# Optimization experiments

Measured on AMD Instinct MI355X. Metric: run time of the kernel, lower is better.

The kernel has to match this reference:

```python
import jax, jax.numpy as jnp
import numpy as np

B, N, C, NQ, DK = 4, 4096, 256, 14, 512
REG, N_ITER = 0.05, 100


def l2norm(x):
    n = jnp.linalg.norm(x, axis=-1, keepdims=True)
    return x / jnp.maximum(n, 1e-12)  # F.normalize(p=2, eps=1e-12)


def sinkhorn(a, b, M, reg=REG, n_iter=N_ITER):
    # a: [B,n] source marginal, b: [B,m] target marginal, M: [B,n,m] cost.
    K = jnp.exp(-M / reg)
    u0 = jnp.ones_like(a) / a.shape[-1]
    v0 = jnp.ones_like(b) / b.shape[-1]
    def step(carry, _):
        u, v = carry
        v = b / (jnp.einsum('bnm,bn->bm', K, u) + 1e-16)
        u = a / (jnp.einsum('bnm,bm->bn', K, v) + 1e-16)
        return (u, v), None
    (u, v), _ = jax.lax.scan(step, (u0, v0), None, length=n_iter)
    return u[:, :, None] * K * v[:, None, :]  # [B,n,m]


def setup_inputs() -> dict:
    key = jax.random.key(0)
    ks = jax.random.split(key, 20)
    s = 0.02
    f32 = jnp.float32
    return {
        'q': jax.random.normal(ks[0], (B, N, C), f32),
        'k': jax.random.normal(ks[1], (B, N, C), f32),
        'v': jax.random.normal(ks[2], (B, N, C), f32),
        'seed_vector': jax.random.normal(ks[3], (B, C, NQ), f32),
        'supp_valid_mask': jax.random.randint(ks[4], (B, N), 0, 2, jnp.int32),
        'supp_mask': jax.random.randint(ks[5], (B, N), 0, 2, jnp.int32),
        'Wq': jax.random.normal(ks[6], (C, C), f32) * s,
        'Wk': jax.random.normal(ks[7], (C, C), f32) * s,
        'Wv': jax.random.normal(ks[8], (C, C), f32) * s,
        'Ws': jax.random.normal(ks[9], (C, C), f32) * s,
        'Wsq': jax.random.normal(ks[10], (C, C), f32) * s,
        'Wsk': jax.random.normal(ks[11], (C, C), f32) * s,
        'Wproj': jax.random.normal(ks[12], (C, C), f32) * s,
        'Wqs': jax.random.normal(ks[13], (C, DK), f32) * s,
        'Wks': jax.random.normal(ks[14], (C, DK), f32) * s,
        'Wvs': jax.random.normal(ks[15], (C, DK), f32) * s,
        'Wfc': jax.random.normal(ks[16], (DK, C), f32) * s,
        'bfc': jnp.zeros((C,), f32),
        'ln_g': jnp.ones((C,), f32),
        'ln_b': jnp.zeros((C,), f32),
    }


def reference(q, k, v, seed_vector, supp_valid_mask, supp_mask,
              Wq, Wk, Wv, Ws, Wsq, Wsk, Wproj, Wqs, Wks, Wvs, Wfc, bfc, ln_g, ln_b):
    # ---- input projections (eval mode: all dropouts are identity) ----
    qs = q @ Wq                                   # [B,N,C]
    kk = k @ Wk                                   # [B,N,C]
    vv = v @ Wv                                   # [B,N,C]
    seed = jnp.einsum('bcq,cd->bqd', seed_vector, Ws)  # s_fc(seed.permute) -> [B,NQ,C]

    # ---- MultiHeadAttentionOne (n_head=1, d_k=d_v=512) ----
    qh = seed @ Wqs                               # [B,NQ,DK]
    kh = kk @ Wks                                 # [B,N,DK]
    vh = vv @ Wvs                                 # [B,N,DK]
    logits = jnp.einsum('bqd,bnd->bqn', qh, kh) / jnp.sqrt(jnp.float32(DK))
    logits = jnp.where(supp_mask[:, None, :] == 0, jnp.float32(-1e9), logits)
    A = jax.nn.softmax(logits, axis=-1)
    ctx = jnp.einsum('bqn,bnd->bqd', A, vh) @ Wfc + bfc  # [B,NQ,C]
    pre = ctx + seed                              # residual
    mu = jnp.mean(pre, axis=-1, keepdims=True)
    var = jnp.var(pre, axis=-1, keepdims=True)
    prototypes = (pre - mu) / jnp.sqrt(var + 1e-5) * ln_g + ln_b  # [B,NQ,C]

    pk = prototypes @ Wsk                         # seed_k_fc
    pq = prototypes @ Wsq                         # seed_q_fc

    # ---- cosine similarity q->prototypes ----
    att_q2p = jnp.einsum('bnc,bkc->bnk', l2norm(qs), l2norm(pk))  # [B,N,NQ]

    # ---- OT-enhanced similarity supp->prototypes ----
    att = jnp.einsum('bnc,bkc->bnk', l2norm(kk), l2norm(pq))      # [B,N,NQ]
    num_bg = jnp.sum((supp_mask == 0).astype(jnp.float32), axis=-1, keepdims=True)  # [B,1]
    num_fg = jnp.float32(N) - num_bg
    trash = jnp.where((supp_mask > 0)[:, :, None], jnp.float32(2.0), jnp.float32(0.0))  # [B,N,1]
    cost = jnp.concatenate([1.0 - att, trash], axis=2)            # [B,N,NQ+1]
    col = jnp.full((B, N), 1.0 / N, dtype=jnp.float32)
    row = jnp.concatenate([jnp.broadcast_to(num_fg / NQ, (B, NQ)), num_bg], axis=1) / N
    T = sinkhorn(col, row, cost) * N
    att_s2p = jax.nn.relu(T[:, :, :-1])                           # [B,N,NQ]

    sid_s = jnp.argmax(att_s2p, axis=2)                           # [B,N] int
    sid_q = jnp.argmax(att_q2p, axis=2)                           # [B,N] int

    attn = jnp.einsum('bnk,bmk->bnm', att_q2p, att_s2p)           # [B,Nq,Nk]

    # ---- align mask (vectorized form of the per-batch loop) ----
    align = jnp.sqrt((sid_s.astype(jnp.float32) + 1.5)[:, :, None] *
                     (sid_q.astype(jnp.float32) + 1.5)[:, None, :])  # [B,Nk,Nq]
    not_align = jnp.where((2.0 * align) % 1.0 == 0.0, 0.0, 1.0)
    not_align = jnp.transpose(not_align, (0, 2, 1))               # [B,Nq,Nk]

    attn = attn + supp_valid_mask[:, None, :].astype(jnp.float32) * (-10000.0)
    attn = attn + not_align * (-10000.0)
    attn = jax.nn.softmax(attn, axis=-1)
    x = (attn @ vv) @ Wproj                                       # [B,N,C]
    return x
```

## Files before the change

### kernel.cpp

```cpp
#include <hip/hip_runtime.h>
#include <math.h>

#define NB 4
#define NN 4096
#define NC 256
#define NQ 14

typedef __attribute__((ext_vector_type(8))) short short8;
typedef __attribute__((ext_vector_type(4))) float f32x4;
typedef _Float16 f16x8 __attribute__((ext_vector_type(8)));
union UH8 { uint4 u4; f16x8 h8; _Float16 h[8]; };

__device__ __forceinline__ float blockReduceSum256(float v, float* sred) {
    #pragma unroll
    for (int off = 32; off; off >>= 1) v += __shfl_xor(v, off, 64);
    const int lane = threadIdx.x & 63, wid = threadIdx.x >> 6;
    if (lane == 0) sred[wid] = v;
    __syncthreads();
    float s = sred[0] + sred[1] + sred[2] + sred[3];
    __syncthreads();
    return s;
}

__device__ __forceinline__ float dpp_wave_sum63(float x) {
    x += __int_as_float(__builtin_amdgcn_update_dpp(0, __float_as_int(x), 0x111, 0xf, 0xf, true));
    x += __int_as_float(__builtin_amdgcn_update_dpp(0, __float_as_int(x), 0x112, 0xf, 0xf, true));
    x += __int_as_float(__builtin_amdgcn_update_dpp(0, __float_as_int(x), 0x114, 0xf, 0xf, true));
    x += __int_as_float(__builtin_amdgcn_update_dpp(0, __float_as_int(x), 0x118, 0xf, 0xf, true));
    x += __int_as_float(__builtin_amdgcn_update_dpp(0, __float_as_int(x), 0x142, 0xf, 0xf, true));
    x += __int_as_float(__builtin_amdgcn_update_dpp(0, __float_as_int(x), 0x143, 0xf, 0xf, true));
    return x;
}
__device__ __forceinline__ float rdlane(float x, int l) {
    return __int_as_float(__builtin_amdgcn_readlane(__float_as_int(x), l));
}

__global__ __launch_bounds__(256) void gemm_aw(const float* __restrict__ A,
                                               const float* __restrict__ W,
                                               float* __restrict__ out) {
    const int t = threadIdx.x;
    const int row0 = blockIdx.y * 64;
    const int cb = blockIdx.x * 128;
    __shared__ __align__(16) float Ast[32][68];
    __shared__ __align__(16) float Wt[32][132];
    const int r0 = (t & 15) * 4;
    const int c0 = (t >> 4) * 8;
    const int ar = t >> 2;
    const int ak = (t & 3) * 8;
    const int wr = t >> 3;
    const int wc = (t & 7) * 16;
    float acc[4][8];
    #pragma unroll
    for (int i = 0; i < 4; i++)
        #pragma unroll
        for (int j = 0; j < 8; j++) acc[i][j] = 0.f;

    for (int k0 = 0; k0 < 256; k0 += 32) {
        const float* asrc = A + (size_t)(row0 + ar) * 256 + k0 + ak;
        float4 a0 = *(const float4*)asrc;
        float4 a1 = *(const float4*)(asrc + 4);
        const float* wsrc = W + (size_t)(k0 + wr) * 256 + cb + wc;
        float4 w0 = *(const float4*)wsrc;
        float4 w1 = *(const float4*)(wsrc + 4);
        float4 w2 = *(const float4*)(wsrc + 8);
        float4 w3 = *(const float4*)(wsrc + 12);
        __syncthreads();
        Ast[ak + 0][ar] = a0.x; Ast[ak + 1][ar] = a0.y;
        Ast[ak + 2][ar] = a0.z; Ast[ak + 3][ar] = a0.w;
        Ast[ak + 4][ar] = a1.x; Ast[ak + 5][ar] = a1.y;
        Ast[ak + 6][ar] = a1.z; Ast[ak + 7][ar] = a1.w;
        *(float4*)&Wt[wr][wc + 0] = w0;
        *(float4*)&Wt[wr][wc + 4] = w1;
        *(float4*)&Wt[wr][wc + 8] = w2;
        *(float4*)&Wt[wr][wc + 12] = w3;
        __syncthreads();
        #pragma unroll
        for (int kk = 0; kk < 32; kk++) {
            const float4 a4 = *(const float4*)&Ast[kk][r0];
            const float4 wa = *(const float4*)&Wt[kk][c0];
            const float4 wb = *(const float4*)&Wt[kk][c0 + 4];
            const float av[4] = {a4.x, a4.y, a4.z, a4.w};
            const float wv[8] = {wa.x, wa.y, wa.z, wa.w, wb.x, wb.y, wb.z, wb.w};
            #pragma unroll
            for (int i = 0; i < 4; i++)
                #pragma unroll
                for (int j = 0; j < 8; j++) acc[i][j] += av[i] * wv[j];
        }
    }
    #pragma unroll
    for (int i = 0; i < 4; i++) {
        float* dst = out + (size_t)(row0 + r0 + i) * 256 + cb + c0;
        *(float4*)dst = make_float4(acc[i][0], acc[i][1], acc[i][2], acc[i][3]);
        *(float4*)(dst + 4) = make_float4(acc[i][4], acc[i][5], acc[i][6], acc[i][7]);
    }
}

__global__ __launch_bounds__(256) void prep_wqk(const float* __restrict__ Wqs,
                                                const float* __restrict__ Wks,
                                                float* __restrict__ Wqk2) {
    __shared__ __align__(16) float srow[512];
    const int c1 = blockIdx.x, c2 = threadIdx.x;
    srow[c2] = Wqs[c1 * 512 + c2];
    srow[c2 + 256] = Wqs[c1 * 512 + 256 + c2];
    __syncthreads();
    const float* wk = Wks + (size_t)c2 * 512;
    float acc = 0.f;
    for (int d = 0; d < 512; d += 4) {
        float4 a = *(const float4*)&srow[d];
        float4 b = *(const float4*)(wk + d);
        acc += a.x * b.x + a.y * b.y + a.z * b.z + a.w * b.w;
    }
    Wqk2[c1 * 256 + c2] = acc * 0.044194173824159216f;
}

__global__ __launch_bounds__(256) void prep_wcomb(const float* __restrict__ Wvs,
                                                  const float* __restrict__ Wfc,
                                                  float* __restrict__ Wcomb) {
    __shared__ float srow[512];
    const int c1 = blockIdx.x, c2 = threadIdx.x;
    srow[c2] = Wvs[c1 * 512 + c2];
    srow[c2 + 256] = Wvs[c1 * 512 + 256 + c2];
    __syncthreads();
    float acc = 0.f;
    for (int d = 0; d < 512; d++) acc += srow[d] * Wfc[d * 256 + c2];
    Wcomb[c1 * 256 + c2] = acc;
}

__global__ __launch_bounds__(256) void k_seed(const float* __restrict__ sv,
                                              const float* __restrict__ Ws,
                                              const float* __restrict__ Wqk2,
                                              float* __restrict__ seed,
                                              float* __restrict__ qhk) {
    const int q = blockIdx.x, b = blockIdx.y, c = threadIdx.x;
    __shared__ float ssv[256];
    __shared__ float sseed[256];
    ssv[c] = sv[((size_t)b * 256 + c) * 14 + q];
    __syncthreads();
    float acc = 0.f;
    for (int d = 0; d < 256; d++) acc += ssv[d] * Ws[d * 256 + c];
    seed[((size_t)b * 14 + q) * 256 + c] = acc;
    sseed[c] = acc;
    __syncthreads();
    float a2 = 0.f;
    for (int d = 0; d < 256; d++) a2 += sseed[d] * Wqk2[d * 256 + c];
    qhk[((size_t)b * 14 + q) * 256 + c] = a2;
}

__global__ __launch_bounds__(256) void k_vvhalf(const float* __restrict__ vv,
                                                _Float16* __restrict__ vvT_h) {
    __shared__ float tile[64][65];
    const int b = blockIdx.z, c0 = blockIdx.y * 64, m0 = blockIdx.x * 64;
    const int t = threadIdx.x;
    #pragma unroll
    for (int i = 0; i < 4; i++) {
        const int m = (t >> 4) + i * 16;
        const float4 v4 = *(const float4*)(vv + ((size_t)b * 4096 + m0 + m) * 256 + c0 + (t & 15) * 4);
        tile[(t & 15) * 4 + 0][m] = v4.x;
        tile[(t & 15) * 4 + 1][m] = v4.y;
        tile[(t & 15) * 4 + 2][m] = v4.z;
        tile[(t & 15) * 4 + 3][m] = v4.w;
    }
    __syncthreads();
    const int c = t >> 2, mo = (t & 3) * 16;
    UH8 o0, o1;
    #pragma unroll
    for (int j = 0; j < 8; j++) {
        o0.h[j] = (_Float16)tile[c][mo + j];
        o1.h[j] = (_Float16)tile[c][mo + 8 + j];
    }
    const size_t off = ((size_t)b * 256 + c0 + c) * 4096 + m0 + mo;
    *(uint4*)(vvT_h + off) = o0.u4;
    *(uint4*)(vvT_h + off + 8) = o1.u4;
}

__global__ __launch_bounds__(256) void k_logits1(const float* __restrict__ kk,
                                                 const float* __restrict__ qhk,
                                                 const int* __restrict__ supp,
                                                 float* __restrict__ logits) {
    const int b = blockIdx.y;
    const int n = blockIdx.x * 256 + threadIdx.x;
    __shared__ __align__(16) float sq[14][256];
    for (int i = threadIdx.x; i < 14 * 256; i += 256) sq[i >> 8][i & 255] = qhk[b * 14 * 256 + i];
    __syncthreads();
    float acc[14];
    #pragma unroll
    for (int q = 0; q < 14; q++) acc[q] = 0.f;
    const float* krow = kk + ((size_t)b * 4096 + n) * 256;
    for (int c = 0; c < 256; c += 4) {
        const float4 k4 = *(const float4*)(krow + c);
        #pragma unroll
        for (int q = 0; q < 14; q++) {
            const float4 a4 = *(const float4*)&sq[q][c];
            acc[q] += k4.x * a4.x + k4.y * a4.y + k4.z * a4.z + k4.w * a4.w;
        }
    }
    const bool msk = (supp[b * 4096 + n] == 0);
    #pragma unroll
    for (int q = 0; q < 14; q++)
        logits[((size_t)b * 14 + q) * 4096 + n] = msk ? -1e9f : acc[q];
}

__global__ __launch_bounds__(256) void k_softmax1(float* __restrict__ logits) {
    const int b = blockIdx.y, qq = blockIdx.x, t = threadIdx.x;
    __shared__ __align__(16) float sl[4096];
    __shared__ float sred[8];
    float* row = logits + ((size_t)b * 14 + qq) * 4096;
    float mx = -3e38f;
    for (int i = t; i < 4096; i += 256) { float v = row[i]; sl[i] = v; mx = fmaxf(mx, v); }
    #pragma unroll
    for (int off = 32; off; off >>= 1) mx = fmaxf(mx, __shfl_xor(mx, off, 64));
    if ((t & 63) == 0) sred[t >> 6] = mx;
    __syncthreads();
    mx = fmaxf(fmaxf(sred[0], sred[1]), fmaxf(sred[2], sred[3]));
    __syncthreads();
    float s = 0.f;
    for (int i = t; i < 4096; i += 256) { float e = expf(sl[i] - mx); sl[i] = e; s += e; }
    #pragma unroll
    for (int off = 32; off; off >>= 1) s += __shfl_xor(s, off, 64);
    if ((t & 63) == 0) sred[t >> 6] = s;
    __syncthreads();
    s = sred[0] + sred[1] + sred[2] + sred[3];
    const float inv = 1.f / s;
    for (int i = t; i < 4096; i += 256) row[i] = sl[i] * inv;
}

__global__ __launch_bounds__(256) void k_ctxv(const float* __restrict__ A,
                                              const float* __restrict__ vv,
                                              float* __restrict__ part) {
    const int b = blockIdx.y, ch = blockIdx.x, c = threadIdx.x;
    const int n0 = ch * 256;
    __shared__ __align__(16) float sA[14][256];
    for (int i = c; i < 14 * 256; i += 256) {
        int qq = i >> 8, j = i & 255;
        sA[qq][j] = A[((size_t)b * 14 + qq) * 4096 + n0 + j];
    }
    __syncthreads();
    float acc[14];
    #pragma unroll
    for (int q = 0; q < 14; q++) acc[q] = 0.f;
    for (int n = 0; n < 256; n += 4) {
        const float v0 = vv[((size_t)b * 4096 + n0 + n + 0) * 256 + c];
        const float v1 = vv[((size_t)b * 4096 + n0 + n + 1) * 256 + c];
        const float v2 = vv[((size_t)b * 4096 + n0 + n + 2) * 256 + c];
        const float v3 = vv[((size_t)b * 4096 + n0 + n + 3) * 256 + c];
        #pragma unroll
        for (int q = 0; q < 14; q++) {
            const float4 a4 = *(const float4*)&sA[q][n];
            acc[q] += a4.x * v0 + a4.y * v1 + a4.z * v2 + a4.w * v3;
        }
    }
    #pragma unroll
    for (int q = 0; q < 14; q++) part[(((size_t)b * 16 + ch) * 14 + q) * 256 + c] = acc[q];
}

__global__ __launch_bounds__(256) void k_proto(const float* __restrict__ part,
                                               const float* __restrict__ Wcomb,
                                               const float* __restrict__ bfc,
                                               const float* __restrict__ seed,
                                               const float* __restrict__ lng,
                                               const float* __restrict__ lnb,
                                               const float* __restrict__ Wsk,
                                               const float* __restrict__ Wsq,
                                               float* __restrict__ pkn,
                                               float* __restrict__ pqn) {
    const int q = blockIdx.x, b = blockIdx.y, c = threadIdx.x;
    __shared__ float sctx[256];
    __shared__ float sproto[256];
    __shared__ float sred[8];
    float cv = 0.f;
    for (int ch = 0; ch < 16; ch++) cv += part[(((size_t)b * 16 + ch) * 14 + q) * 256 + c];
    sctx[c] = cv;
    __syncthreads();
    float pre = 0.f;
    for (int d = 0; d < 256; d++) pre += sctx[d] * Wcomb[d * 256 + c];
    pre += bfc[c] + seed[((size_t)b * 14 + q) * 256 + c];
    const float mu = blockReduceSum256(pre, sred) * (1.f / 256.f);
    const float dv = pre - mu;
    const float var = blockReduceSum256(dv * dv, sred) * (1.f / 256.f);
    const float proto = dv * (1.f / sqrtf(var + 1e-5f)) * lng[c] + lnb[c];
    sproto[c] = proto;
    __syncthreads();
    float pk = 0.f, pq = 0.f;
    for (int d = 0; d < 256; d++) {
        const float sp = sproto[d];
        pk += sp * Wsk[d * 256 + c];
        pq += sp * Wsq[d * 256 + c];
    }
    const float nk = blockReduceSum256(pk * pk, sred);
    const float nq = blockReduceSum256(pq * pq, sred);
    pkn[((size_t)b * 14 + q) * 256 + c] = pk / fmaxf(sqrtf(nk), 1e-12f);
    pqn[((size_t)b * 14 + q) * 256 + c] = pq / fmaxf(sqrtf(nq), 1e-12f);
}

__global__ __launch_bounds__(256) void k_q2p(const float* __restrict__ qs,
                                             const float* __restrict__ kk,
                                             const float* __restrict__ pkn,
                                             const float* __restrict__ pqn,
                                             float* __restrict__ aq2p,
                                             float* __restrict__ attc,
                                             int* __restrict__ sidq) {
    const int b = blockIdx.y;
    const int n = blockIdx.x * 256 + threadIdx.x;
    __shared__ __align__(16) float spk[14][256];
    __shared__ __align__(16) float spq[14][256];
    for (int i = threadIdx.x; i < 14 * 256; i += 256) {
        spk[i >> 8][i & 255] = pkn[b * 14 * 256 + i];
        spq[i >> 8][i & 255] = pqn[b * 14 * 256 + i];
    }
    __syncthreads();
    float aq[14], ak[14];
    #pragma unroll
    for (int q = 0; q < 14; q++) { aq[q] = 0.f; ak[q] = 0.f; }
    float nq = 0.f, nk = 0.f;
    const float* qrow = qs + ((size_t)b * 4096 + n) * 256;
    const float* krow = kk + ((size_t)b * 4096 + n) * 256;
    for (int c = 0; c < 256; c += 4) {
        const float4 q4 = *(const float4*)(qrow + c);
        const float4 k4 = *(const float4*)(krow + c);
        nq += q4.x * q4.x + q4.y * q4.y + q4.z * q4.z + q4.w * q4.w;
        nk += k4.x * k4.x + k4.y * k4.y + k4.z * k4.z + k4.w * k4.w;
        #pragma unroll
        for (int q = 0; q < 14; q++) {
            const float4 p4 = *(const float4*)&spk[q][c];
            const float4 p4b = *(const float4*)&spq[q][c];
            aq[q] += q4.x * p4.x + q4.y * p4.y + q4.z * p4.z + q4.w * p4.w;
            ak[q] += k4.x * p4b.x + k4.y * p4b.y + k4.z * p4b.z + k4.w * p4b.w;
        }
    }
    const float sq_ = 1.f / fmaxf(sqrtf(nq), 1e-12f);
    const float sk_ = 1.f / fmaxf(sqrtf(nk), 1e-12f);
    float* aqrow = aq2p + ((size_t)b * 4096 + n) * 14;
    float* akrow = attc + ((size_t)b * 4096 + n) * 14;
    int best = 0;
    float bv = -3e38f;
    #pragma unroll
    for (int q = 0; q < 14; q++) {
        const float v = aq[q] * sq_;
        aqrow[q] = v;
        if (v > bv) { bv = v; best = q; }
        akrow[q] = ak[q] * sk_;
    }
    sidq[b * 4096 + n] = best;
}

__global__ __launch_bounds__(512, 1) void k_sinkhorn(const float* __restrict__ attc,
                                                     const int* __restrict__ supp,
                                                     const int* __restrict__ valid,
                                                     _Float16* __restrict__ as2ph,
                                                     int* __restrict__ code) {
    const int b = blockIdx.x;
    const int t = threadIdx.x;
    const int lane = t & 63, wid = t >> 6;
    __shared__ __align__(16) float wred[2][15][8];
    __shared__ float sbg[8];
    float K[8][15], u[8];
    float bgcnt = 0.f;
    #pragma unroll
    for (int j = 0; j < 8; j++) {
        const int n = t + j * 512;
        const int sm = supp[b * 4096 + n];
        bgcnt += (sm == 0) ? 1.f : 0.f;
        const float* arow = attc + ((size_t)b * 4096 + n) * 14;
        #pragma unroll
        for (int m = 0; m < 14; m++) K[j][m] = expf(-20.f * (1.f - arow[m]));
        K[j][14] = (sm > 0) ? expf(-40.f) : 1.f;
        u[j] = 1.f / 4096.f;
    }
    #pragma unroll
    for (int j = 0; j < 8; j++)
        #pragma unroll
        for (int m = 0; m < 15; m++)
            asm volatile("" : "+v"(K[j][m]));
    const float bgw = dpp_wave_sum63(bgcnt);
    if (lane == 63) sbg[wid] = bgw;
    __syncthreads();
    float num_bg = 0.f;
    #pragma unroll
    for (int w = 0; w < 8; w++) num_bg += sbg[w];
    const float num_fg = 4096.f - num_bg;
    const float bm_fg = num_fg / (14.f * 4096.f);
    const float bm_tr = num_bg / 4096.f;
    const float a_n = 1.f / 4096.f;
    const float mybm = (lane < 14) ? bm_fg : bm_tr;

    float vloc[15];
    for (int it = 0; it < 100; it++) {
        const int buf = it & 1;
        float tot[15];
        #pragma unroll
        for (int m = 0; m < 15; m++) {
            float s = 0.f;
            #pragma unroll
            for (int j = 0; j < 8; j++) s += K[j][m] * u[j];
            tot[m] = rdlane(dpp_wave_sum63(s), 63);
        }
        float wv = 0.f;
        #pragma unroll
        for (int m = 0; m < 15; m++) wv = (lane == m) ? tot[m] : wv;
        if (lane < 15) wred[buf][lane][wid] = wv;
        __syncthreads();
        float vtmp = 0.f;
        {
            const float4 r0 = *(const float4*)&wred[buf][lane < 15 ? lane : 0][0];
            const float4 r1 = *(const float4*)&wred[buf][lane < 15 ? lane : 0][4];
            const float s = r0.x + r0.y + r0.z + r0.w + r1.x + r1.y + r1.z + r1.w;
            vtmp = mybm * __builtin_amdgcn_rcpf(s + 1e-16f);
        }
        #pragma unroll
        for (int m = 0; m < 15; m++) vloc[m] = rdlane(vtmp, m);
        #pragma unroll
        for (int j = 0; j < 8; j++) {
            float s = 0.f;
            #pragma unroll
            for (int m = 0; m < 15; m++) s += K[j][m] * vloc[m];
            u[j] = a_n * __builtin_amdgcn_rcpf(s + 1e-16f);
        }
    }
    #pragma unroll
    for (int j = 0; j < 8; j++) {
        const int n = t + j * 512;
        float bv = -3e38f;
        int bi = 0;
        union { uint4 u4[4]; _Float16 h[32]; } ob;
        #pragma unroll
        for (int m = 0; m < 14; m++) {
            const float tv = fmaxf(4096.f * u[j] * K[j][m] * vloc[m], 0.f);
            const _Float16 hh = (_Float16)tv;
            ob.h[m] = hh;
            ob.h[16 + m] = (_Float16)(tv - (float)hh);
            if (tv > bv) { bv = tv; bi = m; }
        }
        ob.h[14] = (_Float16)0.f; ob.h[15] = (_Float16)0.f;
        ob.h[30] = (_Float16)0.f; ob.h[31] = (_Float16)0.f;
        uint4* dst = (uint4*)(as2ph + ((size_t)(b * 4096 + n)) * 32);
        dst[0] = ob.u4[0]; dst[1] = ob.u4[1];
        dst[2] = ob.u4[2]; dst[3] = ob.u4[3];
        int msk = 1 << bi;
        if (bi == 0) msk |= (1 << 12);
        else if (bi == 12) msk |= 1;
        else if (bi == 3) msk |= (1 << 11);
        else if (bi == 11) msk |= (1 << 3);
        code[b * 4096 + n] = msk | (valid[b * 4096 + n] << 14);
    }
}

__global__ __launch_bounds__(256) void k_lamtab(const int* __restrict__ code,
                                                int* __restrict__ lamtab) {
    const int b = blockIdx.x, t = threadIdx.x;
    __shared__ int sm0[4], sm1[4];
    int m0 = 0, m1 = 0;
    for (int m = t; m < 4096; m += 256) {
        const int c = code[b * 4096 + m];
        const int mask = c & 0x3fff;
        const int v = c >> 14;
        const int nmask = (~mask) & 0x3fff;
        if (v == 0) { m0 |= mask; m1 |= nmask; }
        else { m1 |= mask; }
    }
    #pragma unroll
    for (int off = 32; off; off >>= 1) {
        m0 |= __shfl_xor(m0, off, 64);
        m1 |= __shfl_xor(m1, off, 64);
    }
    if ((t & 63) == 0) { sm0[t >> 6] = m0; sm1[t >> 6] = m1; }
    __syncthreads();
    if (t == 0) {
        lamtab[b * 2 + 0] = sm0[0] | sm0[1] | sm0[2] | sm0[3];
        lamtab[b * 2 + 1] = sm1[0] | sm1[1] | sm1[2] | sm1[3];
    }
}

__global__ __launch_bounds__(512, 2) void k_fused(const float* __restrict__ aq2p,
                                                  const _Float16* __restrict__ as2ph,
                                                  const int* __restrict__ code,
                                                  const int* __restrict__ sidq,
                                                  const int* __restrict__ lamtab,
                                                  const _Float16* __restrict__ vvT_h,
                                                  float* __restrict__ y) {
    const int bid = blockIdx.x;
    const int xcd = bid & 7, slot = bid >> 3;
    const int b = xcd >> 1;
    const int n0 = ((xcd & 1) * 64 + slot) * 32;
    const int t = threadIdx.x;
    const int l = t & 63, wv = t >> 6;
    const int wn = wv & 1, wcS = wv >> 1;
    const int quad = l >> 4, lr = l & 15;

    __shared__ __align__(16) _Float16 Pl[2][32 * 128];
    __shared__ float rsl[4][32];
    __shared__ int ssq[32], sml[32];
    __shared__ float rinv_s[32];

    if (t < 32) {
        const int sq = sidq[b * 4096 + n0 + t];
        const int lm0 = lamtab[b * 2], lm1 = lamtab[b * 2 + 1];
        ssq[t] = sq;
        sml[t] = ((lm0 >> sq) & 1) ? 0 : (((lm1 >> sq) & 1) ? 1 : 2);
    }
    __syncthreads();
    int sqp = 0;
    #pragma unroll
    for (int r = 0; r < 4; r++) {
        const int row_l = wn * 16 + quad * 4 + r;
        sqp |= (ssq[row_l] & 31) << (r * 8);
        sqp |= (sml[row_l] & 3) << (r * 8 + 5);
    }
    UH8 a1, a2;
    {
        const float* arow = aq2p + ((size_t)(b * 4096 + n0 + wn * 16 + lr)) * 14;
        const int kb = (quad & 1) * 8;
        #pragma unroll
        for (int j = 0; j < 8; j++) {
            const int kk2 = kb + j;
            const float f = (kk2 < 14) ? arow[kk2] : 0.f;
            const _Float16 hi = (_Float16)f;
            a1.h[j] = hi;
            a2.h[j] = (quad < 2) ? (_Float16)(f - (float)hi) : (_Float16)0.f;
        }
    }
    const _Float16* a2base = as2ph + (size_t)b * 4096 * 32 + quad * 8;
    const int* cbase = code + b * 4096;
    const _Float16* bvb0 = vvT_h + ((size_t)(b * 256 + wv * 32 + lr)) * 4096 + quad * 8;
    const _Float16* bvb1 = bvb0 + (size_t)16 * 4096;

    UH8 bS[2];
    int cdr[2];
    #pragma unroll
    for (int i = 0; i < 2; i++) {
        const int m = (wcS * 2 + i) * 16 + lr;
        bS[i].u4 = *(const uint4*)(a2base + (size_t)m * 32);
        cdr[i] = cbase[m];
    }
    UH8 bA[8], bB[8];
    #pragma unroll
    for (int ms = 0; ms < 4; ms++) {
        bA[ms * 2 + 0].u4 = *(const uint4*)(bvb0 + ms * 32);
        bA[ms * 2 + 1].u4 = *(const uint4*)(bvb1 + ms * 32);
    }
    f32x4 acc[2][2];
    #pragma unroll
    for (int fr = 0; fr < 2; fr++)
        #pragma unroll
        for (int ct = 0; ct < 2; ct++) acc[fr][ct] = (f32x4){0.f, 0.f, 0.f, 0.f};
    float rs4[4] = {0.f, 0.f, 0.f, 0.f};

#define FCHUNK(CUR, NXT, CH, LAST)                                             \
  {                                                                            \
    _Float16* PlW = Pl[(CH) & 1];                                              \
    _Pragma("unroll")                                                          \
    for (int i = 0; i < 2; i++) {                                              \
      f32x4 S = (f32x4){0.f, 0.f, 0.f, 0.f};                                   \
      S = __builtin_amdgcn_mfma_f32_16x16x32_f16(a1.h8, bS[i].h8, S, 0, 0, 0); \
      S = __builtin_amdgcn_mfma_f32_16x16x32_f16(a2.h8, bS[i].h8, S, 0, 0, 0); \
      const int cd = cdr[i];                                                   \
      const int mlocal = (wcS * 2 + i) * 16 + lr;                              \
      _Pragma("unroll")                                                        \
      for (int r = 0; r < 4; r++) {                                            \
        const int sq_r = (sqp >> (r * 8)) & 31;                                \
        const int ml_r = (sqp >> (r * 8 + 5)) & 3;                             \
        const int lvl = (cd >> 14) + 1 - ((cd >> sq_r) & 1);                   \
        const float p = (lvl == ml_r) ? __expf(S[r]) : 0.f;                    \
        rs4[r] += p;                                                           \
        const int nrow = wn * 16 + quad * 4 + r;                               \
        PlW[nrow * 128 + (mlocal ^ ((nrow & 7) << 3))] = (_Float16)p;          \
      }                                                                        \
    }                                                                          \
    if (!(LAST)) {                                                             \
      const int mcn = ((CH) + 1) * 128;                                        \
      _Pragma("unroll")                                                        \
      for (int i = 0; i < 2; i++) {                                            \
        const int m = mcn + (wcS * 2 + i) * 16 + lr;                           \
        bS[i].u4 = *(const uint4*)(a2base + (size_t)m * 32);                   \
        cdr[i] = cbase[m];                                                     \
      }                                                                        \
      _Pragma("unroll")                                                        \
      for (int ms = 0; ms < 4; ms++) {                                         \
        NXT[ms * 2 + 0].u4 = *(const uint4*)(bvb0 + mcn + ms * 32);            \
        NXT[ms * 2 + 1].u4 = *(const uint4*)(bvb1 + mcn + ms * 32);            \
      }                                                                        \
    }                                                                          \
    asm volatile("s_waitcnt lgkmcnt(0)" ::: "memory");                         \
    __builtin_amdgcn_s_barrier();                                              \
    asm volatile("" ::: "memory");                                             \
    const _Float16* PlR = Pl[(CH) & 1];                                        \
    __builtin_amdgcn_s_setprio(1);                                             \
    _Pragma("unroll")                                                          \
    for (int ms = 0; ms < 4; ms++) {                                           \
      UH8 aP0, aP1;                                                            \
      const int mb = ms * 32 + quad * 8;                                       \
      const int msw = mb ^ ((lr & 7) << 3);                                    \
      aP0.u4 = *(const uint4*)&PlR[lr * 128 + msw];                            \
      aP1.u4 = *(const uint4*)&PlR[(16 + lr) * 128 + msw];                     \
      acc[0][0] = __builtin_amdgcn_mfma_f32_16x16x32_f16(aP0.h8, CUR[ms * 2 + 0].h8, acc[0][0], 0, 0, 0); \
      acc[0][1] = __builtin_amdgcn_mfma_f32_16x16x32_f16(aP0.h8, CUR[ms * 2 + 1].h8, acc[0][1], 0, 0, 0); \
      acc[1][0] = __builtin_amdgcn_mfma_f32_16x16x32_f16(aP1.h8, CUR[ms * 2 + 0].h8, acc[1][0], 0, 0, 0); \
      acc[1][1] = __builtin_amdgcn_mfma_f32_16x16x32_f16(aP1.h8, CUR[ms * 2 + 1].h8, acc[1][1], 0, 0, 0); \
    }                                                                          \
    __builtin_amdgcn_s_setprio(0);                                             \
  }

    #pragma unroll 1
    for (int ch2 = 0; ch2 < 16; ch2++) {
        FCHUNK(bA, bB, ch2 * 2, false);
        FCHUNK(bB, bA, ch2 * 2 + 1, (ch2 == 15));
    }
#undef FCHUNK

    #pragma unroll
    for (int r = 0; r < 4; r++) {
        float v = rs4[r];
        v += __shfl_xor(v, 1, 64);
        v += __shfl_xor(v, 2, 64);
        v += __shfl_xor(v, 4, 64);
        v += __shfl_xor(v, 8, 64);
        rs4[r] = v;
    }
    __syncthreads();
    if (lr == 0) {
        #pragma unroll
        for (int r = 0; r < 4; r++) rsl[wcS][wn * 16 + quad * 4 + r] = rs4[r];
    }
    __syncthreads();
    if (t < 32) rinv_s[t] = 1.f / (rsl[0][t] + rsl[1][t] + rsl[2][t] + rsl[3][t]);
    __syncthreads();
    #pragma unroll
    for (int fr = 0; fr < 2; fr++)
        #pragma unroll
        for (int ct = 0; ct < 2; ct++)
            #pragma unroll
            for (int j = 0; j < 4; j++) {
                const int rowd = fr * 16 + quad * 4 + j;
                y[((size_t)b * 4096 + n0 + rowd) * 256 + wv * 32 + ct * 16 + lr] =
                    acc[fr][ct][j] * rinv_s[rowd];
            }
}

extern "C" void kernel_launch(void* const* d_in, const int* in_sizes, int n_in,
                              void* d_out, int out_size, void* d_ws, size_t ws_size,
                              hipStream_t stream) {
    (void)in_sizes; (void)n_in; (void)out_size; (void)ws_size;
    const float* q    = (const float*)d_in[0];
    const float* k    = (const float*)d_in[1];
    const float* v    = (const float*)d_in[2];
    const float* sv   = (const float*)d_in[3];
    const int*  valid = (const int*)d_in[4];
    const int*  supp  = (const int*)d_in[5];
    const float* Wq   = (const float*)d_in[6];
    const float* Wk   = (const float*)d_in[7];
    const float* Wv   = (const float*)d_in[8];
    const float* Ws   = (const float*)d_in[9];
    const float* Wsq  = (const float*)d_in[10];
    const float* Wsk  = (const float*)d_in[11];
    const float* Wproj= (const float*)d_in[12];
    const float* Wqs  = (const float*)d_in[13];
    const float* Wks  = (const float*)d_in[14];
    const float* Wvs  = (const float*)d_in[15];
    const float* Wfc  = (const float*)d_in[16];
    const float* bfc  = (const float*)d_in[17];
    const float* lng  = (const float*)d_in[18];
    const float* lnb  = (const float*)d_in[19];

    float* ws = (float*)d_ws;
    _Float16* as2ph = (_Float16*)ws;
    float* qs   = ws + 0;
    float* kk   = ws + 4194304;
    float* vv   = ws + 8388608;
    float* y0   = ws + 33554432;
    float* wqk2 = ws + 37748736;
    float* wcomb= ws + 37814272;
    float* seed = ws + 37879808;
    float* qhk  = ws + 37894144;
    float* logA = ws + 37908480;
    float* cpart= ws + 38137856;
    float* pkn  = ws + 38367232;
    float* pqn  = ws + 38381568;
    float* aq2p = ws + 38395904;
    float* attc = ws + 38625280;
    int* code   = (int*)(ws + 39084032);
    int* sidq   = (int*)(ws + 39100416);
    int* lamtab = (int*)(ws + 39116800);
    _Float16* vvT_h = (_Float16*)(ws + 39133216);

    gemm_aw<<<dim3(2, 256), 256, 0, stream>>>(q, Wq, qs);
    gemm_aw<<<dim3(2, 256), 256, 0, stream>>>(k, Wk, kk);
    gemm_aw<<<dim3(2, 256), 256, 0, stream>>>(v, Wv, vv);
    k_vvhalf<<<dim3(64, 4, 4), 256, 0, stream>>>(vv, vvT_h);
    prep_wqk<<<256, 256, 0, stream>>>(Wqs, Wks, wqk2);
    prep_wcomb<<<256, 256, 0, stream>>>(Wvs, Wfc, wcomb);
    k_seed<<<dim3(14, 4), 256, 0, stream>>>(sv, Ws, wqk2, seed, qhk);
    k_logits1<<<dim3(16, 4), 256, 0, stream>>>(kk, qhk, supp, logA);
    k_softmax1<<<dim3(14, 4), 256, 0, stream>>>(logA);
    k_ctxv<<<dim3(16, 4), 256, 0, stream>>>(logA, vv, cpart);
    k_proto<<<dim3(14, 4), 256, 0, stream>>>(cpart, wcomb, bfc, seed, lng, lnb, Wsk, Wsq, pkn, pqn);
    k_q2p<<<dim3(16, 4), 256, 0, stream>>>(qs, kk, pkn, pqn, aq2p, attc, sidq);
    k_sinkhorn<<<4, 512, 0, stream>>>(attc, supp, valid, as2ph, code);
    k_lamtab<<<4, 256, 0, stream>>>(code, lamtab);
    k_fused<<<dim3(512), 512, 0, stream>>>(aq2p, as2ph, code, sidq, lamtab, vvT_h, y0);
    gemm_aw<<<dim3(2, 256), 256, 0, stream>>>(y0, Wproj, (float*)d_out);
}
```

Before: 781.7 us.

## Replace FP32 SIMT projection GEMMs with split-fp16 MFMA GEMMs

The four 256x256 projection GEMMs move from an LDS-tiled fp32 FMA kernel to MFMA 16x16x32 f16 instructions. Each operand is split into hi/lo fp16 parts and three MFMAs per tile keep near-fp32 accuracy. Weights are pre-transposed and split by a new prep kernel into workspace buffers that are reused later. This adds extra launches and drops LDS staging, so A and W are read directly from global memory.

Result: slower. 825.2 us (+5.6%).

```diff
diff --git a/kernel.cpp b/kernel.cpp
--- a/kernel.cpp
+++ b/kernel.cpp
@@ -35,64 +35,56 @@
     return __int_as_float(__builtin_amdgcn_readlane(__float_as_int(x), l));
 }
 
-__global__ __launch_bounds__(256) void gemm_aw(const float* __restrict__ A,
-                                               const float* __restrict__ W,
+__global__ __launch_bounds__(256) void prep_wT(const float* __restrict__ W,
+                                               _Float16* __restrict__ WT) {
+    const int col = blockIdx.x, t = threadIdx.x;
+    const float f = W[(size_t)t * 256 + col];
+    const _Float16 hi = (_Float16)f;
+    WT[(size_t)col * 256 + t] = hi;
+    WT[65536 + (size_t)col * 256 + t] = (_Float16)(f - (float)hi);
+}
+
+__global__ __launch_bounds__(256) void gemm_mf(const float* __restrict__ A,
+                                               const _Float16* __restrict__ WT,
                                                float* __restrict__ out) {
     const int t = threadIdx.x;
-    const int row0 = blockIdx.y * 64;
-    const int cb = blockIdx.x * 128;
-    __shared__ __align__(16) float Ast[32][68];
-    __shared__ __align__(16) float Wt[32][132];
-    const int r0 = (t & 15) * 4;
-    const int c0 = (t >> 4) * 8;
-    const int ar = t >> 2;
-    const int ak = (t & 3) * 8;
-    const int wr = t >> 3;
-    const int wc = (t & 7) * 16;
-    float acc[4][8];
-    #pragma unroll
-    for (int i = 0; i < 4; i++)
-        #pragma unroll
-        for (int j = 0; j < 8; j++) acc[i][j] = 0.f;
-
+    const int w = t >> 6, l = t & 63;
+    const int quad = l >> 4, lr = l & 15;
+    const int row0 = blockIdx.y * 64 + w * 16;
+    const int cb = blockIdx.x * 64;
+    const float* arow = A + (size_t)(row0 + lr) * 256;
+    const _Float16* wth = WT + (size_t)(cb + lr) * 256 + quad * 8;
+    const _Float16* wtl = wth + 65536;
+    f32x4 acc[4];
+    #pragma unroll
+    for (int ct = 0; ct < 4; ct++) acc[ct] = (f32x4){0.f, 0.f, 0.f, 0.f};
+    #pragma unroll
     for (int k0 = 0; k0 < 256; k0 += 32) {
-        const float* asrc = A + (size_t)(row0 + ar) * 256 + k0 + ak;
-        float4 a0 = *(const float4*)asrc;
-        float4 a1 = *(const float4*)(asrc + 4);
-        const float* wsrc = W + (size_t)(k0 + wr) * 256 + cb + wc;
-        float4 w0 = *(const float4*)wsrc;
-        float4 w1 = *(const float4*)(wsrc + 4);
-        float4 w2 = *(const float4*)(wsrc + 8);
-        float4 w3 = *(const float4*)(wsrc + 12);
-        __syncthreads();
-        Ast[ak + 0][ar] = a0.x; Ast[ak + 1][ar] = a0.y;
-        Ast[ak + 2][ar] = a0.z; Ast[ak + 3][ar] = a0.w;
-        Ast[ak + 4][ar] = a1.x; Ast[ak + 5][ar] = a1.y;
-        Ast[ak + 6][ar] = a1.z; Ast[ak + 7][ar] = a1.w;
-        *(float4*)&Wt[wr][wc + 0] = w0;
-        *(float4*)&Wt[wr][wc + 4] = w1;
-        *(float4*)&Wt[wr][wc + 8] = w2;
-        *(float4*)&Wt[wr][wc + 12] = w3;
-        __syncthreads();
-        #pragma unroll
-        for (int kk = 0; kk < 32; kk++) {
-            const float4 a4 = *(const float4*)&Ast[kk][r0];
-            const float4 wa = *(const float4*)&Wt[kk][c0];
-            const float4 wb = *(const float4*)&Wt[kk][c0 + 4];
-            const float av[4] = {a4.x, a4.y, a4.z, a4.w};
-            const float wv[8] = {wa.x, wa.y, wa.z, wa.w, wb.x, wb.y, wb.z, wb.w};
-            #pragma unroll
-            for (int i = 0; i < 4; i++)
-                #pragma unroll
-                for (int j = 0; j < 8; j++) acc[i][j] += av[i] * wv[j];
-        }
-    }
-    #pragma unroll
-    for (int i = 0; i < 4; i++) {
-        float* dst = out + (size_t)(row0 + r0 + i) * 256 + cb + c0;
-        *(float4*)dst = make_float4(acc[i][0], acc[i][1], acc[i][2], acc[i][3]);
-        *(float4*)(dst + 4) = make_float4(acc[i][4], acc[i][5], acc[i][6], acc[i][7]);
-    }
+        const float4 f0 = *(const float4*)(arow + k0 + quad * 8);
+        const float4 f1 = *(const float4*)(arow + k0 + quad * 8 + 4);
+        UH8 a1, a2;
+        const float fv[8] = {f0.x, f0.y, f0.z, f0.w, f1.x, f1.y, f1.z, f1.w};
+        #pragma unroll
+        for (int j = 0; j < 8; j++) {
+            const _Float16 hi = (_Float16)fv[j];
+            a1.h[j] = hi;
+            a2.h[j] = (_Float16)(fv[j] - (float)hi);
+        }
+        #pragma unroll
+        for (int ct = 0; ct < 4; ct++) {
+            UH8 bh, bl;
+            bh.u4 = *(const uint4*)(wth + (size_t)ct * 4096 + k0);
+            bl.u4 = *(const uint4*)(wtl + (size_t)ct * 4096 + k0);
+            acc[ct] = __builtin_amdgcn_mfma_f32_16x16x32_f16(a1.h8, bh.h8, acc[ct], 0, 0, 0);
+            acc[ct] = __builtin_amdgcn_mfma_f32_16x16x32_f16(a2.h8, bh.h8, acc[ct], 0, 0, 0);
+            acc[ct] = __builtin_amdgcn_mfma_f32_16x16x32_f16(a1.h8, bl.h8, acc[ct], 0, 0, 0);
+        }
+    }
+    #pragma unroll
+    for (int ct = 0; ct < 4; ct++)
+        #pragma unroll
+        for (int r = 0; r < 4; r++)
+            out[(size_t)(row0 + quad * 4 + r) * 256 + cb + ct * 16 + lr] = acc[ct][r];
 }
 
 __global__ __launch_bounds__(256) void prep_wqk(const float* __restrict__ Wqs,
@@ -680,10 +672,17 @@
     int* sidq   = (int*)(ws + 39100416);
     int* lamtab = (int*)(ws + 39116800);
     _Float16* vvT_h = (_Float16*)(ws + 39133216);
-
-    gemm_aw<<<dim3(2, 256), 256, 0, stream>>>(q, Wq, qs);
-    gemm_aw<<<dim3(2, 256), 256, 0, stream>>>(k, Wk, kk);
-    gemm_aw<<<dim3(2, 256), 256, 0, stream>>>(v, Wv, vv);
+    _Float16* WqT = (_Float16*)logA;
+    _Float16* WkT = (_Float16*)cpart;
+    _Float16* WvT = (_Float16*)attc;
+    _Float16* WpT = (_Float16*)logA;
+
+    prep_wT<<<256, 256, 0, stream>>>(Wq, WqT);
+    prep_wT<<<256, 256, 0, stream>>>(Wk, WkT);
+    prep_wT<<<256, 256, 0, stream>>>(Wv, WvT);
+    gemm_mf<<<dim3(4, 256), 256, 0, stream>>>(q, WqT, qs);
+    gemm_mf<<<dim3(4, 256), 256, 0, stream>>>(k, WkT, kk);
+    gemm_mf<<<dim3(4, 256), 256, 0, stream>>>(v, WvT, vv);
     k_vvhalf<<<dim3(64, 4, 4), 256, 0, stream>>>(vv, vvT_h);
     prep_wqk<<<256, 256, 0, stream>>>(Wqs, Wks, wqk2);
     prep_wcomb<<<256, 256, 0, stream>>>(Wvs, Wfc, wcomb);
@@ -691,10 +690,11 @@
     k_logits1<<<dim3(16, 4), 256, 0, stream>>>(kk, qhk, supp, logA);
     k_softmax1<<<dim3(14, 4), 256, 0, stream>>>(logA);
     k_ctxv<<<dim3(16, 4), 256, 0, stream>>>(logA, vv, cpart);
+    prep_wT<<<256, 256, 0, stream>>>(Wproj, WpT);
     k_proto<<<dim3(14, 4), 256, 0, stream>>>(cpart, wcomb, bfc, seed, lng, lnb, Wsk, Wsq, pkn, pqn);
     k_q2p<<<dim3(16, 4), 256, 0, stream>>>(qs, kk, pkn, pqn, aq2p, attc, sidq);
     k_sinkhorn<<<4, 512, 0, stream>>>(attc, supp, valid, as2ph, code);
     k_lamtab<<<4, 256, 0, stream>>>(code, lamtab);
     k_fused<<<dim3(512), 512, 0, stream>>>(aq2p, as2ph, code, sidq, lamtab, vvT_h, y0);
-    gemm_aw<<<dim3(2, 256), 256, 0, stream>>>(y0, Wproj, (float*)d_out);
-}
+    gemm_mf<<<dim3(4, 256), 256, 0, stream>>>(y0, WpT, (float*)d_out);
+}
```
